# Kernel optimization log

Measured on AMD Instinct MI355X. Metric: run time of the kernel, lower is better.

Reference implementation:

```python
import jax, jax.numpy as jnp
import numpy as np

TRNA_N, DIS_N = 8000, 6000
D, H, E, B = 128, 256, 320000, 16384
NEG_SLOPE = 0.2  # gat_alpha
TEMP = 0.5


def _gat(src, tgt, s_idx, t_idx, Wsrc, Wtgt, a, n_src):
    # BipartiteGraphAttentionLayer (eval mode, dropout off)
    h_i = src @ Wsrc.T            # [n_src, D]
    h_j = tgt @ Wtgt.T            # [n_tgt, D]
    # cat([h_i[s], h_j[t]]) @ a == (h_i @ a[:D])[s] + (h_j @ a[D:])[t]
    s_i = h_i @ a[:D]             # [n_src]
    s_j = h_j @ a[D:]             # [n_tgt]
    e = jax.nn.leaky_relu(s_i[s_idx] + s_j[t_idx], NEG_SLOPE)
    e = jnp.clip(e, -30.0, 30.0)
    exp_e = jnp.exp(e)
    denom = jax.ops.segment_sum(exp_e, s_idx, num_segments=n_src)
    alpha = exp_e / (denom[s_idx] + 1e-8)
    out = jax.ops.segment_sum(h_j[t_idx] * alpha[:, None], s_idx, num_segments=n_src)
    return jax.nn.elu(out)


def _hg(x, S):
    # HCCF-style parameter-free hypergraph conv: nodes -> hyperedges -> nodes
    return jax.nn.elu(S @ (S.T @ x))


def _info_nce(z1, z2):
    z1 = z1 / (jnp.linalg.norm(z1, axis=1, keepdims=True) + 1e-12)
    z2 = z2 / (jnp.linalg.norm(z2, axis=1, keepdims=True) + 1e-12)
    sim = (z1 @ z2.T) / TEMP      # [N, N]
    logp = jax.nn.log_softmax(sim, axis=1)
    return -jnp.mean(jnp.diagonal(logp))


def setup_inputs():
    key = jax.random.key(0)
    ks = jax.random.split(key, 20)
    xn = lambda k, shp, sc: jax.random.normal(k, shp, dtype=jnp.float32) * sc
    d2 = (2.0 / (2 * D)) ** 0.5
    return dict(
        trna_embed=xn(ks[0], (TRNA_N, D), (2.0 / (TRNA_N + D)) ** 0.5),
        disease_embed=xn(ks[1], (DIS_N, D), (2.0 / (DIS_N + D)) ** 0.5),
        thyper=xn(ks[2], (D, H), (2.0 / (D + H)) ** 0.5),
        dhyper=xn(ks[3], (D, H), (2.0 / (D + H)) ** 0.5),
        gat_t_Wsrc=xn(ks[4], (3, D, D), d2),
        gat_t_Wtgt=xn(ks[5], (3, D, D), d2),
        gat_t_a=xn(ks[6], (3, 2 * D), 1.414 * (2.0 / (2 * D + 1)) ** 0.5),
        gat_d_Wsrc=xn(ks[7], (3, D, D), d2),
        gat_d_Wtgt=xn(ks[8], (3, D, D), d2),
        gat_d_a=xn(ks[9], (3, 2 * D), 1.414 * (2.0 / (2 * D + 1)) ** 0.5),
        mlp_W1=xn(ks[10], (D, 2 * D), (2.0 / (3 * D)) ** 0.5),
        mlp_b1=jnp.zeros((D,), jnp.float32),
        mlp_W2=xn(ks[11], (1, D), (2.0 / (D + 1)) ** 0.5),
        mlp_b2=jnp.zeros((1,), jnp.float32),
        gate_W=xn(ks[12], (1, D), (2.0 / (D + 1)) ** 0.5),
        gate_b=jnp.zeros((1,), jnp.float32),
        src_id=jax.random.randint(ks[13], (E,), 0, TRNA_N),
        tgt_id=jax.random.randint(ks[14], (E,), 0, DIS_N),
        trna_ids=jax.random.randint(ks[15], (B,), 0, TRNA_N),
        disease_ids=jax.random.randint(ks[16], (B,), 0, DIS_N),
    )


def reference(trna_embed, disease_embed, thyper, dhyper,
              gat_t_Wsrc, gat_t_Wtgt, gat_t_a,
              gat_d_Wsrc, gat_d_Wtgt, gat_d_a,
              mlp_W1, mlp_b1, mlp_W2, mlp_b2, gate_W, gate_b,
              src_id, tgt_id, trna_ids, disease_ids):
    # stage 1: simple-graph GAT pass
    sg_t = _gat(trna_embed, disease_embed, src_id, tgt_id,
                gat_t_Wsrc[0], gat_t_Wtgt[0], gat_t_a[0], TRNA_N)
    sg_d = _gat(disease_embed, sg_t, tgt_id, src_id,
                gat_d_Wsrc[0], gat_d_Wtgt[0], gat_d_a[0], DIS_N)
    # hypergraph passes 1-2
    hg_t = _hg(sg_t, sg_t @ thyper)
    hg_d = _hg(sg_d, sg_d @ dhyper)
    hg_t = _hg(hg_t, hg_t @ thyper)
    hg_d = _hg(hg_d, hg_d @ dhyper)
    # GAT layers 2-3 on hypergraph outputs
    sg_t = _gat(hg_t, hg_d, src_id, tgt_id,
                gat_t_Wsrc[1], gat_t_Wtgt[1], gat_t_a[1], TRNA_N)
    sg_d = _gat(hg_d, hg_t, tgt_id, src_id,
                gat_d_Wsrc[1], gat_d_Wtgt[1], gat_d_a[1], DIS_N)
    sg_t = _gat(sg_t, sg_d, src_id, tgt_id,
                gat_t_Wsrc[2], gat_t_Wtgt[2], gat_t_a[2], TRNA_N)
    sg_d = _gat(sg_d, sg_t, tgt_id, src_id,
                gat_d_Wsrc[2], gat_d_Wtgt[2], gat_d_a[2], DIS_N)
    # hypergraph pass 3
    hg_t = _hg(hg_t, hg_t @ thyper)
    hg_d = _hg(hg_d, hg_d @ dhyper)
    final_t = sg_t + hg_t
    final_d = sg_d + hg_d
    sel_t = final_t[trna_ids]
    sel_d = final_d[disease_ids]
    contrast = _info_nce(sg_t, hg_t) + _info_nce(sg_d, hg_d)
    gmf_vec = sel_t * sel_d
    gmf_pred = jnp.sum(gmf_vec, axis=-1)
    mlp_in = jnp.concatenate([sel_t, sel_d], axis=-1)
    h1 = jax.nn.relu(mlp_in @ mlp_W1.T + mlp_b1)
    mlp_pred = (h1 @ mlp_W2.T + mlp_b2)[:, 0]
    gate = jax.nn.sigmoid(gmf_vec @ gate_W.T + gate_b)[:, 0]
    fusion_pred = gate * gmf_pred + (1.0 - gate) * mlp_pred
    return (fusion_pred, sg_t, sg_d, gmf_pred, mlp_pred, contrast)
```

## Files before the change

### kernel.cpp

```cpp
#include <hip/hip_runtime.h>
#include <math.h>

#define N_T 8000
#define N_D 6000
#define N_E 320000
#define N_B 16384
#define NSTRIP 8

typedef __attribute__((ext_vector_type(8))) short s16x8;
typedef __attribute__((ext_vector_type(8))) __bf16 bf16x8;
typedef __attribute__((ext_vector_type(4))) float f32x4;

static __device__ __forceinline__ f32x4 mfma16(s16x8 a, s16x8 b, f32x4 c) {
  return __builtin_amdgcn_mfma_f32_16x16x32_bf16(
      __builtin_bit_cast(bf16x8, a), __builtin_bit_cast(bf16x8, b), c, 0, 0, 0);
}

static __device__ __forceinline__ unsigned short f2bf(float f) {
  unsigned u = __float_as_uint(f);
  u += 0x7FFF + ((u >> 16) & 1);
  return (unsigned short)(u >> 16);
}

static __device__ __forceinline__ float bf2f(unsigned short u) {
  return __uint_as_float(((unsigned)u) << 16);
}

__device__ __forceinline__ float wave_sum(float v) {
  v += __shfl_xor(v, 32, 64);
  v += __shfl_xor(v, 16, 64);
  v += __shfl_xor(v, 8, 64);
  v += __shfl_xor(v, 4, 64);
  v += __shfl_xor(v, 2, 64);
  v += __shfl_xor(v, 1, 64);
  return v;
}

__device__ __forceinline__ float half_sum(float v) {
  v += __shfl_xor(v, 16, 64);
  v += __shfl_xor(v, 8, 64);
  v += __shfl_xor(v, 4, 64);
  v += __shfl_xor(v, 2, 64);
  v += __shfl_xor(v, 1, 64);
  return v;
}

__global__ void k_hist2(const int* __restrict__ src, const int* __restrict__ tgt,
                        int* __restrict__ cnt) {
  int i = blockIdx.x * 256 + threadIdx.x;
  if (i < N_E) atomicAdd(&cnt[src[i]], 1);
  else if (i < 2 * N_E) atomicAdd(&cnt[N_T + tgt[i - N_E]], 1);
}

__global__ void k_scan2(const int* __restrict__ cnt, int* __restrict__ rp_t,
    int* __restrict__ cur_t, int* __restrict__ rp_d, int* __restrict__ cur_d) {
  const int* c = blockIdx.x ? cnt + N_T : cnt;
  const int n = blockIdx.x ? N_D : N_T;
  int* rp = blockIdx.x ? rp_d : rp_t;
  int* cur = blockIdx.x ? cur_d : cur_t;
  __shared__ int buf[1024];
  __shared__ int carry_s;
  if (threadIdx.x == 0) carry_s = 0;
  __syncthreads();
  for (int base = 0; base < n; base += 1024) {
    int c0 = carry_s;
    int i = base + (int)threadIdx.x;
    int v = (i < n) ? c[i] : 0;
    buf[threadIdx.x] = v;
    __syncthreads();
    for (int off = 1; off < 1024; off <<= 1) {
      int t = (threadIdx.x >= (unsigned)off) ? buf[threadIdx.x - off] : 0;
      __syncthreads();
      buf[threadIdx.x] += t;
      __syncthreads();
    }
    int incl = buf[threadIdx.x];
    if (i < n) { int e = c0 + incl - v; rp[i] = e; cur[i] = e; }
    __syncthreads();
    if (threadIdx.x == 0) carry_s = c0 + buf[1023];
    __syncthreads();
  }
  if (threadIdx.x == 0) rp[n] = carry_s;
}

__global__ void k_scatter2(const int* __restrict__ src, const int* __restrict__ tgt,
    int* __restrict__ cur_t, int* __restrict__ cur_d,
    int* __restrict__ nbr_t, int* __restrict__ nbr_d) {
  int i = blockIdx.x * 256 + threadIdx.x;
  if (i < N_E) {
    int p = atomicAdd(&cur_t[src[i]], 1);
    nbr_t[p] = tgt[i];
  } else if (i < 2 * N_E) {
    i -= N_E;
    int p = atomicAdd(&cur_d[tgt[i]], 1);
    nbr_d[p] = src[i];
  }
}

__global__ __launch_bounds__(256) void k_pgemm(const float* __restrict__ th,
    const float* __restrict__ dh, float* __restrict__ P_t, float* __restrict__ P_d) {
  const float* A = blockIdx.x < 4 ? th : dh;
  float* C = blockIdx.x < 4 ? P_t : P_d;
  const int sub = blockIdx.x & 3;
  const int row0 = (sub >> 1) * 64, col0 = (sub & 1) * 64;
  __shared__ float As[16][65];
  __shared__ float Bs[16][65];
  const int tid = threadIdx.x;
  const int tr = tid >> 4, tc = tid & 15;
  float acc[4][4] = {};
  for (int k0 = 0; k0 < 256; k0 += 16) {
    {
      int m = tid >> 2, kk = (tid & 3) * 4;
      float4 v = *(const float4*)(A + (size_t)(row0 + m) * 256 + k0 + kk);
      As[kk + 0][m] = v.x; As[kk + 1][m] = v.y; As[kk + 2][m] = v.z; As[kk + 3][m] = v.w;
    }
    {
      int nn = tid >> 2, kk = (tid & 3) * 4;
      float4 v = *(const float4*)(A + (size_t)(col0 + nn) * 256 + k0 + kk);
      Bs[kk + 0][nn] = v.x; Bs[kk + 1][nn] = v.y; Bs[kk + 2][nn] = v.z; Bs[kk + 3][nn] = v.w;
    }
    __syncthreads();
#pragma unroll
    for (int k = 0; k < 16; ++k) {
      float a[4], b[4];
#pragma unroll
      for (int i = 0; i < 4; ++i) a[i] = As[k][tr * 4 + i];
#pragma unroll
      for (int j = 0; j < 4; ++j) b[j] = Bs[k][tc * 4 + j];
#pragma unroll
      for (int i = 0; i < 4; ++i)
#pragma unroll
        for (int j = 0; j < 4; ++j)
          acc[i][j] = fmaf(a[i], b[j], acc[i][j]);
    }
    __syncthreads();
  }
#pragma unroll
  for (int i = 0; i < 4; ++i)
#pragma unroll
    for (int j = 0; j < 4; ++j)
      C[(size_t)(row0 + tr * 4 + i) * 128 + col0 + tc * 4 + j] = acc[i][j];
}

__global__ void k_tobf16m(const float* __restrict__ a0, unsigned short* __restrict__ y0,
    const float* __restrict__ a1, unsigned short* __restrict__ y1,
    const float* __restrict__ a2, unsigned short* __restrict__ y2,
    const float* __restrict__ a3, unsigned short* __restrict__ y3) {
  int i = blockIdx.x * 256 + threadIdx.x;
  const float* x; unsigned short* y;
  if (i < 12288) { x = a0; y = y0; }
  else if (i < 24576) { x = a1; y = y1; i -= 12288; }
  else if (i < 32768) { x = a2; y = y2; i -= 24576; }
  else if (i < 224768) { x = a3; y = y3; i -= 32768; }
  else return;
  float4 v = ((const float4*)x)[i];
  ushort4 o;
  o.x = f2bf(v.x); o.y = f2bf(v.y); o.z = f2bf(v.z); o.w = f2bf(v.w);
  ((ushort4*)y)[i] = o;
}

template<int K, int ACT, int BIAS, int SJMODE, int OUTF, int OUTB>
static __device__ __forceinline__ void mfma_body(
    const unsigned short* __restrict__ A, const unsigned short* __restrict__ B,
    const float* __restrict__ bias, const float* __restrict__ a2,
    float* __restrict__ Cf, unsigned short* __restrict__ Cb,
    float* __restrict__ sj_out, int M, int bx) {
  const int wave = threadIdx.x >> 6, lane = threadIdx.x & 63;
  const int row0 = bx * 32;
  const int col0 = wave * 32;
  const int l15 = lane & 15, kg = lane >> 4;
  constexpr int NS = K / 32;
  f32x4 acc[2][2] = {};
  s16x8 ab[2][2], bb[2][2];
  auto ld = [&](int buf, int k0) {
#pragma unroll
    for (int i = 0; i < 2; ++i) {
      int r = row0 + i * 16 + l15;
      ab[buf][i] = (r < M) ? *(const s16x8*)(A + (size_t)r * K + k0 + kg * 8) : (s16x8)0;
    }
#pragma unroll
    for (int j = 0; j < 2; ++j) {
      int c = col0 + j * 16 + l15;
      bb[buf][j] = *(const s16x8*)(B + (size_t)c * K + k0 + kg * 8);
    }
  };
  ld(0, 0);
#pragma unroll
  for (int s = 0; s < NS; ++s) {
    if (s + 1 < NS) ld((s + 1) & 1, (s + 1) * 32);
#pragma unroll
    for (int i = 0; i < 2; ++i)
#pragma unroll
      for (int j = 0; j < 2; ++j)
        acc[i][j] = mfma16(ab[s & 1][i], bb[s & 1][j], acc[i][j]);
  }
  __shared__ float sjl[4][32];
  float a2v[2];
  if (SJMODE) {
#pragma unroll
    for (int j = 0; j < 2; ++j) a2v[j] = a2[col0 + j * 16 + l15];
  }
#pragma unroll
  for (int i = 0; i < 2; ++i) {
    float part[4] = {0.f, 0.f, 0.f, 0.f};
#pragma unroll
    for (int j = 0; j < 2; ++j) {
      int gc = col0 + j * 16 + l15;
      float bv = BIAS ? bias[gc] : 0.f;
#pragma unroll
      for (int r = 0; r < 4; ++r) {
        int gr = row0 + i * 16 + kg * 4 + r;
        float v = acc[i][j][r] + bv;
        if (SJMODE == 1) part[r] += v * a2v[j];
        if (ACT == 1) v = v > 0.f ? v : __expf(v) - 1.f;
        if (ACT == 2) v = fmaxf(v, 0.f);
        if (SJMODE == 2) part[r] += v * a2v[j];
        if (gr < M) {
          if (OUTF) Cf[(size_t)gr * 128 + gc] = v;
          if (OUTB) Cb[(size_t)gr * 128 + gc] = f2bf(v);
        }
      }
    }
    if (SJMODE) {
#pragma unroll
      for (int r = 0; r < 4; ++r) {
        float p = part[r];
        p += __shfl_xor(p, 1, 64);
        p += __shfl_xor(p, 2, 64);
        p += __shfl_xor(p, 4, 64);
        p += __shfl_xor(p, 8, 64);
        if (l15 == 0) sjl[wave][i * 16 + kg * 4 + r] = p;
      }
    }
  }
  if (SJMODE) {
    __syncthreads();
    if (threadIdx.x < 32) {
      int gr = row0 + (int)threadIdx.x;
      if (gr < M)
        sj_out[gr] = sjl[0][threadIdx.x] + sjl[1][threadIdx.x] +
                     sjl[2][threadIdx.x] + sjl[3][threadIdx.x];
    }
  }
}

template<int K, int ACT, int BIAS, int SJMODE, int OUTF, int OUTB>
__global__ __launch_bounds__(256) void k_mfma(const unsigned short* __restrict__ A,
    const unsigned short* __restrict__ B, const float* __restrict__ bias,
    const float* __restrict__ a2, float* __restrict__ Cf, unsigned short* __restrict__ Cb,
    float* __restrict__ sj_out, int M) {
  mfma_body<K, ACT, BIAS, SJMODE, OUTF, OUTB>(A, B, bias, a2, Cf, Cb, sj_out, M, blockIdx.x);
}

template<int K, int ACT, int SJMODE, int OUTF, int OUTB>
__global__ __launch_bounds__(256) void k_mfma2(
    const unsigned short* __restrict__ A0, const unsigned short* __restrict__ B0,
    const float* __restrict__ a20, float* __restrict__ Cf0,
    unsigned short* __restrict__ Cb0, float* __restrict__ sj0, int M0, int G0,
    const unsigned short* __restrict__ A1, const unsigned short* __restrict__ B1,
    const float* __restrict__ a21, float* __restrict__ Cf1,
    unsigned short* __restrict__ Cb1, float* __restrict__ sj1, int M1) {
  int bx = blockIdx.x;
  if (bx < G0)
    mfma_body<K, ACT, 0, SJMODE, OUTF, OUTB>(A0, B0, nullptr, a20, Cf0, Cb0, sj0, M0, bx);
  else
    mfma_body<K, ACT, 0, SJMODE, OUTF, OUTB>(A1, B1, nullptr, a21, Cf1, Cb1, sj1, M1, bx - G0);
}

__global__ __launch_bounds__(256) void k_nce3(
    const unsigned short* __restrict__ z1t, const unsigned short* __restrict__ z2t,
    float* __restrict__ rs_tp,
    const unsigned short* __restrict__ z1d, const unsigned short* __restrict__ z2d,
    float* __restrict__ rs_dp) {
  __shared__ unsigned short bt[128 * 128];
  const int wave = threadIdx.x >> 6, lane = threadIdx.x & 63;
  const int l15 = lane & 15, kg = lane >> 4;
  int by = blockIdx.y;
  const unsigned short *z1, *z2; float* rowsum; int M, N;
  if (by < 63) { z1 = z1t; z2 = z2t; rowsum = rs_tp; M = N_T; N = N_T; }
  else { by -= 63; z1 = z1d; z2 = z2d; rowsum = rs_dp; M = N_D; N = N_D; }
  const int row0 = by * 128 + (wave >> 1) * 64;
  const int colw = (wave & 1) * 64;
  const int CT = (N + 127) >> 7;
  const int ctps = (CT + NSTRIP - 1) / NSTRIP;
  const int ct0 = blockIdx.x * ctps;
  const int ct1 = min(CT, ct0 + ctps);
  if (ct0 >= CT) return;
  s16x8 a[4][4];
#pragma unroll
  for (int ks = 0; ks < 4; ++ks)
#pragma unroll
    for (int i = 0; i < 4; ++i) {
      int r = row0 + i * 16 + l15;
      a[ks][i] = (r < M) ? *(const s16x8*)(z1 + (size_t)r * 128 + ks * 32 + kg * 8) : (s16x8)0;
    }
  float rs[4][4] = {};
  for (int ct = ct0; ct < ct1; ++ct) {
    const int cbase = ct * 128;
#pragma unroll
    for (int i = 0; i < 8; ++i) {
      int c = i * 256 + (int)threadIdx.x;
      int trow = c >> 4, ks = c & 15;
      int rg = cbase + trow;
      rg = rg < N ? rg : N - 1;
      s16x8 v = *(const s16x8*)(z2 + (size_t)rg * 128 + ks * 8);
      *(s16x8*)((char*)bt + trow * 256 + ((ks * 16) ^ ((trow & 7) << 4))) = v;
    }
    __syncthreads();
    f32x4 acc[4][4] = {};
#pragma unroll
    for (int ks = 0; ks < 4; ++ks) {
      s16x8 b[4];
#pragma unroll
      for (int j = 0; j < 4; ++j) {
        int trow = colw + j * 16 + l15;
        b[j] = *(const s16x8*)((const char*)bt + trow * 256 +
                               ((ks * 64 + kg * 16) ^ ((trow & 7) << 4)));
      }
#pragma unroll
      for (int i = 0; i < 4; ++i)
#pragma unroll
        for (int j = 0; j < 4; ++j)
          acc[i][j] = mfma16(a[ks][i], b[j], acc[i][j]);
    }
#pragma unroll
    for (int j = 0; j < 4; ++j) {
      int gc = cbase + colw + j * 16 + l15;
      bool cok = gc < N;
#pragma unroll
      for (int i = 0; i < 4; ++i)
#pragma unroll
        for (int r = 0; r < 4; ++r)
          if (cok) rs[i][r] += __expf(acc[i][j][r] * 2.0f);
    }
    __syncthreads();
  }
#pragma unroll
  for (int i = 0; i < 4; ++i)
#pragma unroll
    for (int r = 0; r < 4; ++r) {
      float v = rs[i][r];
      v += __shfl_xor(v, 1, 64);
      v += __shfl_xor(v, 2, 64);
      v += __shfl_xor(v, 4, 64);
      v += __shfl_xor(v, 8, 64);
      if (l15 == 0) {
        int gr = row0 + i * 16 + kg * 4 + r;
        if (gr < M) atomicAdd(&rowsum[gr], v);
      }
    }
}

__global__ __launch_bounds__(256) void k_syrk2m(const unsigned short* __restrict__ xbT,
    const unsigned short* __restrict__ xbD, float* __restrict__ partT,
    float* __restrict__ partD) {
  int b = blockIdx.x;
  const unsigned short* xb; float* part; int n;
  if (b < 128) { xb = xbT; part = partT + (size_t)b * 16384; n = N_T; }
  else { b -= 128; xb = xbD; part = partD + (size_t)b * 16384; n = N_D; }
  __shared__ float rows[4][128];
  int chunk = (n + 127) >> 7;
  int m0 = b * chunk, m1 = min(n, m0 + chunk);
  int tx = threadIdx.x & 15, ty = threadIdx.x >> 4;
  float acc[8][8] = {};
  for (int m = m0; m < m1; m += 4) {
    int nr = min(4, m1 - m);
    if ((int)threadIdx.x < nr * 64) {
      ushort2 u = ((const ushort2*)(xb + (size_t)m * 128))[threadIdx.x];
      rows[threadIdx.x >> 6][(threadIdx.x & 63) * 2] = bf2f(u.x);
      rows[threadIdx.x >> 6][(threadIdx.x & 63) * 2 + 1] = bf2f(u.y);
    }
    __syncthreads();
    for (int r = 0; r < nr; ++r) {
      float a[8], bv[8];
#pragma unroll
      for (int i = 0; i < 8; ++i) a[i] = rows[r][i * 16 + ty];
#pragma unroll
      for (int j = 0; j < 8; ++j) bv[j] = rows[r][j * 16 + tx];
#pragma unroll
      for (int i = 0; i < 8; ++i)
#pragma unroll
        for (int j = 0; j < 8; ++j)
          acc[i][j] = fmaf(a[i], bv[j], acc[i][j]);
    }
    __syncthreads();
  }
#pragma unroll
  for (int i = 0; i < 8; ++i)
#pragma unroll
    for (int j = 0; j < 8; ++j)
      part[(i * 16 + ty) * 128 + j * 16 + tx] = acc[i][j];
}

__global__ void k_redm(const float* __restrict__ partT, const float* __restrict__ partD,
                       float* __restrict__ GmT, float* __restrict__ GmD) {
  int b = blockIdx.x;
  const float* part = b < 64 ? partT : partD;
  float* G = b < 64 ? GmT : GmD;
  int i = (b & 63) * 256 + threadIdx.x;
  float s = 0.f;
  for (int c = 0; c < 128; ++c) s += part[(size_t)c * 16384 + i];
  G[i] = s;
}

__global__ __launch_bounds__(256) void k_wtm(const float* __restrict__ GmT,
    const float* __restrict__ P_t, unsigned short* __restrict__ wb_t,
    const float* __restrict__ GmD, const float* __restrict__ P_d,
    unsigned short* __restrict__ wb_d) {
  const float* G = blockIdx.x < 4 ? GmT : GmD;
  const float* P = blockIdx.x < 4 ? P_t : P_d;
  unsigned short* wb = blockIdx.x < 4 ? wb_t : wb_d;
  const int sub = blockIdx.x & 3;
  const int bi = sub >> 1, bj = sub & 1;
  __shared__ float Gs[64][129];
  __shared__ float Ps[128][65];
  for (int t = threadIdx.x; t < 8192; t += 256) {
    int il = t >> 7, k = t & 127;
    Gs[il][k] = G[(bi * 64 + il) * 128 + k];
    int pk = t >> 6, pj = t & 63;
    Ps[pk][pj] = P[pk * 128 + bj * 64 + pj];
  }
  __syncthreads();
  const int tx = threadIdx.x & 15, ty = threadIdx.x >> 4;
  float acc[4][4] = {};
  for (int k = 0; k < 128; ++k) {
    float a[4], b[4];
#pragma unroll
    for (int i = 0; i < 4; ++i) a[i] = Gs[ty * 4 + i][k];
#pragma unroll
    for (int j = 0; j < 4; ++j) b[j] = Ps[k][tx * 4 + j];
#pragma unroll
    for (int i = 0; i < 4; ++i)
#pragma unroll
      for (int j = 0; j < 4; ++j)
        acc[i][j] = fmaf(a[i], b[j], acc[i][j]);
  }
#pragma unroll
  for (int i = 0; i < 4; ++i)
#pragma unroll
    for (int j = 0; j < 4; ++j)
      wb[(bi * 64 + ty * 4 + i) * 128 + bj * 64 + tx * 4 + j] = f2bf(acc[i][j]);
}

__global__ void k_wvec6(const float* __restrict__ WsT, const float* __restrict__ aT,
                        const float* __restrict__ WsD, const float* __restrict__ aD,
                        float* __restrict__ wv) {
  int b = blockIdx.x, k = threadIdx.x;
  const float* W = b < 3 ? WsT + b * 16384 : WsD + (b - 3) * 16384;
  const float* a = b < 3 ? aT + b * 256 : aD + (b - 3) * 256;
  float s = 0.f;
  for (int n = 0; n < 128; ++n) s = fmaf(W[n * 128 + k], a[n], s);
  wv[b * 128 + k] = s;
}

__global__ void k_rowdot2(const float* __restrict__ trna, const float* __restrict__ dis,
    const float* __restrict__ wv, float* __restrict__ si_ta, float* __restrict__ si_da) {
  int r = blockIdx.x * 4 + (threadIdx.x >> 6);
  int lane = threadIdx.x & 63;
  const float* h; const float* a; float* o; int row;
  if (r < N_T) { h = trna; a = wv; o = si_ta; row = r; }
  else {
    row = r - N_T;
    if (row >= N_D) return;
    h = dis; a = wv + 3 * 128; o = si_da;
  }
  float2 v = *(const float2*)(h + (size_t)row * 128 + lane * 2);
  float2 av = *(const float2*)(a + lane * 2);
  float s = v.x * av.x + v.y * av.y;
  s = wave_sum(s);
  if (lane == 0) o[row] = s;
}

template<int OUTF, int OUTB, int EMIT_SI>
static __device__ __forceinline__ void agg_body(const int* __restrict__ rp,
    const int* __restrict__ nbr, const float* __restrict__ si,
    const float* __restrict__ sj, const unsigned short* __restrict__ hjb,
    float* __restrict__ outF, unsigned short* __restrict__ outB,
    const float* __restrict__ wv, float* __restrict__ si_out, int n, int bx) {
  int r = bx * 8 + ((int)threadIdx.x >> 5);
  int lane = threadIdx.x & 31;
  if (r >= n) return;
  int p0 = rp[r], p1 = rp[r + 1];
  float sir = si[r];
  int c4 = lane * 4;
  auto wcalc = [&](int t) {
    float v = sir + sj[t];
    v = v >= 0.f ? v : 0.2f * v;
    v = fminf(30.f, fmaxf(-30.f, v));
    return __expf(v);
  };
  float a0 = 0.f, a1 = 0.f, a2 = 0.f, a3 = 0.f, den = 0.f;
  int p = p0;
  for (; p + 4 <= p1; p += 4) {
    int t0 = nbr[p], t1 = nbr[p + 1], t2 = nbr[p + 2], t3 = nbr[p + 3];
    float w0 = wcalc(t0), w1 = wcalc(t1), w2 = wcalc(t2), w3 = wcalc(t3);
    ushort4 h0 = *(const ushort4*)(hjb + (size_t)t0 * 128 + c4);
    ushort4 h1 = *(const ushort4*)(hjb + (size_t)t1 * 128 + c4);
    ushort4 h2 = *(const ushort4*)(hjb + (size_t)t2 * 128 + c4);
    ushort4 h3 = *(const ushort4*)(hjb + (size_t)t3 * 128 + c4);
    den += (w0 + w1) + (w2 + w3);
    a0 += w0 * bf2f(h0.x) + w1 * bf2f(h1.x) + w2 * bf2f(h2.x) + w3 * bf2f(h3.x);
    a1 += w0 * bf2f(h0.y) + w1 * bf2f(h1.y) + w2 * bf2f(h2.y) + w3 * bf2f(h3.y);
    a2 += w0 * bf2f(h0.z) + w1 * bf2f(h1.z) + w2 * bf2f(h2.z) + w3 * bf2f(h3.z);
    a3 += w0 * bf2f(h0.w) + w1 * bf2f(h1.w) + w2 * bf2f(h2.w) + w3 * bf2f(h3.w);
  }
  for (; p < p1; ++p) {
    int t = nbr[p];
    float w = wcalc(t);
    ushort4 h = *(const ushort4*)(hjb + (size_t)t * 128 + c4);
    den += w;
    a0 += w * bf2f(h.x); a1 += w * bf2f(h.y);
    a2 += w * bf2f(h.z); a3 += w * bf2f(h.w);
  }
  float inv = 1.0f / (den + 1e-8f);
  float v0 = a0 * inv, v1 = a1 * inv, v2 = a2 * inv, v3 = a3 * inv;
  v0 = v0 > 0.f ? v0 : __expf(v0) - 1.f;
  v1 = v1 > 0.f ? v1 : __expf(v1) - 1.f;
  v2 = v2 > 0.f ? v2 : __expf(v2) - 1.f;
  v3 = v3 > 0.f ? v3 : __expf(v3) - 1.f;
  if (OUTF) {
    float4 of; of.x = v0; of.y = v1; of.z = v2; of.w = v3;
    *(float4*)(outF + (size_t)r * 128 + c4) = of;
  }
  if (OUTB) {
    ushort4 ob; ob.x = f2bf(v0); ob.y = f2bf(v1); ob.z = f2bf(v2); ob.w = f2bf(v3);
    *(ushort4*)(outB + (size_t)r * 128 + c4) = ob;
  }
  if (EMIT_SI) {
    float4 w4 = *(const float4*)(wv + c4);
    float d = v0 * w4.x + v1 * w4.y + v2 * w4.z + v3 * w4.w;
    d += __shfl_xor(d, 16, 64);
    d += __shfl_xor(d, 8, 64);
    d += __shfl_xor(d, 4, 64);
    d += __shfl_xor(d, 2, 64);
    d += __shfl_xor(d, 1, 64);
    if (lane == 0) si_out[r] = d;
  }
}

template<int OUTF, int OUTB, int EMIT_SI>
__global__ __launch_bounds__(256) void k_agg(const int* __restrict__ rp,
    const int* __restrict__ nbr, const float* __restrict__ si,
    const float* __restrict__ sj, const unsigned short* __restrict__ hjb,
    float* __restrict__ outF, unsigned short* __restrict__ outB,
    const float* __restrict__ wv, float* __restrict__ si_out, int n) {
  agg_body<OUTF, OUTB, EMIT_SI>(rp, nbr, si, sj, hjb, outF, outB, wv, si_out, n, blockIdx.x);
}

template<int OUTF, int OUTB, int EMIT_SI>
__global__ __launch_bounds__(256) void k_agg2(
    const int* __restrict__ rp0, const int* __restrict__ nbr0, const float* __restrict__ si0,
    const float* __restrict__ sj0, const unsigned short* __restrict__ hjb0,
    float* __restrict__ outF0, unsigned short* __restrict__ outB0,
    const float* __restrict__ wv0, float* __restrict__ sio0, int n0, int G0,
    const int* __restrict__ rp1, const int* __restrict__ nbr1, const float* __restrict__ si1,
    const float* __restrict__ sj1, const unsigned short* __restrict__ hjb1,
    float* __restrict__ outF1, unsigned short* __restrict__ outB1,
    const float* __restrict__ wv1, float* __restrict__ sio1, int n1) {
  int bx = blockIdx.x;
  if (bx < G0)
    agg_body<OUTF, OUTB, EMIT_SI>(rp0, nbr0, si0, sj0, hjb0, outF0, outB0, wv0, sio0, n0, bx);
  else
    agg_body<OUTF, OUTB, EMIT_SI>(rp1, nbr1, si1, sj1, hjb1, outF1, outB1, wv1, sio1, n1, bx - G0);
}

__global__ void k_norm2(const float* __restrict__ sgt, const float* __restrict__ hgt3,
    const float* __restrict__ sgd, const float* __restrict__ hgd3,
    unsigned short* __restrict__ z1t, unsigned short* __restrict__ z2t,
    unsigned short* __restrict__ z1d, unsigned short* __restrict__ z2d,
    float* __restrict__ rs_t, float* __restrict__ dg_t,
    float* __restrict__ rs_d, float* __restrict__ dg_d) {
  int ridx = blockIdx.x * 4 + (threadIdx.x >> 6);
  int lane = threadIdx.x & 63;
  const float *x1, *x2; unsigned short *o1, *o2; float *rs, *dg; int row;
  if (ridx < 8000) { x1 = sgt; x2 = hgt3; o1 = z1t; o2 = z2t; rs = rs_t; dg = dg_t; row = ridx; }
  else if (ridx < 14000) {
    row = ridx - 8000;
    x1 = sgd; x2 = hgd3; o1 = z1d; o2 = z2d; rs = rs_d; dg = dg_d;
  } else return;
  float2 v1 = *(const float2*)(x1 + (size_t)row * 128 + lane * 2);
  float2 v2 = *(const float2*)(x2 + (size_t)row * 128 + lane * 2);
  float ss1 = wave_sum(v1.x * v1.x + v1.y * v1.y);
  float ss2 = wave_sum(v2.x * v2.x + v2.y * v2.y);
  float i1 = 1.0f / (sqrtf(ss1) + 1e-12f);
  float i2 = 1.0f / (sqrtf(ss2) + 1e-12f);
  float n1x = v1.x * i1, n1y = v1.y * i1;
  float n2x = v2.x * i2, n2y = v2.y * i2;
  ushort2 w1; w1.x = f2bf(n1x); w1.y = f2bf(n1y);
  ushort2 w2; w2.x = f2bf(n2x); w2.y = f2bf(n2y);
  *(ushort2*)(o1 + (size_t)row * 128 + lane * 2) = w1;
  *(ushort2*)(o2 + (size_t)row * 128 + lane * 2) = w2;
  float d = wave_sum(n1x * n2x + n1y * n2y);
  if (lane == 0) { dg[row] = 2.0f * d; rs[row] = 0.f; }
}

__global__ void k_gather(const float* __restrict__ sgt, const float* __restrict__ hgt,
    const float* __restrict__ sgd, const float* __restrict__ hgd,
    const int* __restrict__ tids, const int* __restrict__ dids,
    const float* __restrict__ gateW, unsigned short* __restrict__ mlp_in_b,
    float* __restrict__ gmf, float* __restrict__ gate_lin, int nB) {
  int b = blockIdx.x * 4 + (threadIdx.x >> 6);
  int lane = threadIdx.x & 63;
  if (b >= nB) return;
  int ti = tids[b], di = dids[b];
  float2 a1 = *(const float2*)(sgt + (size_t)ti * 128 + lane * 2);
  float2 a2 = *(const float2*)(hgt + (size_t)ti * 128 + lane * 2);
  float2 c1 = *(const float2*)(sgd + (size_t)di * 128 + lane * 2);
  float2 c2 = *(const float2*)(hgd + (size_t)di * 128 + lane * 2);
  float2 st; st.x = a1.x + a2.x; st.y = a1.y + a2.y;
  float2 sd; sd.x = c1.x + c2.x; sd.y = c1.y + c2.y;
  ushort2 o1; o1.x = f2bf(st.x); o1.y = f2bf(st.y);
  ushort2 o2; o2.x = f2bf(sd.x); o2.y = f2bf(sd.y);
  *(ushort2*)(mlp_in_b + (size_t)b * 256 + lane * 2) = o1;
  *(ushort2*)(mlp_in_b + (size_t)b * 256 + 128 + lane * 2) = o2;
  float2 gv; gv.x = st.x * sd.x; gv.y = st.y * sd.y;
  float2 gw = *(const float2*)(gateW + lane * 2);
  float s1 = gv.x + gv.y;
  float s2 = gv.x * gw.x + gv.y * gw.y;
  s1 = wave_sum(s1);
  s2 = wave_sum(s2);
  if (lane == 0) { gmf[b] = s1; gate_lin[b] = s2; }
}

__global__ void k_final(const float* __restrict__ h1, const float* __restrict__ W2,
    const float* __restrict__ b2, const float* __restrict__ gate_lin,
    const float* __restrict__ gate_b, const float* __restrict__ gmf,
    float* __restrict__ fusion, float* __restrict__ mlp_pred, int nB) {
  int b = blockIdx.x * 4 + (threadIdx.x >> 6);
  int lane = threadIdx.x & 63;
  if (b >= nB) return;
  float2 hv = *(const float2*)(h1 + (size_t)b * 128 + lane * 2);
  float2 wv = *(const float2*)(W2 + lane * 2);
  float s = hv.x * wv.x + hv.y * wv.y;
  s = wave_sum(s);
  if (lane == 0) {
    float mp = s + b2[0];
    float g = 1.0f / (1.0f + __expf(-(gate_lin[b] + gate_b[0])));
    mlp_pred[b] = mp;
    fusion[b] = g * gmf[b] + (1.0f - g) * mp;
  }
}

__global__ void k_contrast(const float* __restrict__ rs_t, const float* __restrict__ dg_t,
    const float* __restrict__ rs_d, const float* __restrict__ dg_d, float* __restrict__ out) {
  __shared__ float red[256];
  float st = 0.f, sd = 0.f;
  for (int i = threadIdx.x; i < N_T; i += 256) st += __logf(rs_t[i]) - dg_t[i];
  for (int i = threadIdx.x; i < N_D; i += 256) sd += __logf(rs_d[i]) - dg_d[i];
  red[threadIdx.x] = st * (1.0f / N_T) + sd * (1.0f / N_D);
  __syncthreads();
  for (int off = 128; off; off >>= 1) {
    if (threadIdx.x < (unsigned)off) red[threadIdx.x] += red[threadIdx.x + off];
    __syncthreads();
  }
  if (threadIdx.x == 0) out[0] = red[0];
}

extern "C" void kernel_launch(void* const* d_in, const int* in_sizes, int n_in,
                              void* d_out, int out_size, void* d_ws, size_t ws_size,
                              hipStream_t stream) {
  const float* trna   = (const float*)d_in[0];
  const float* dis    = (const float*)d_in[1];
  const float* thyper = (const float*)d_in[2];
  const float* dhyper = (const float*)d_in[3];
  const float* WsrcT  = (const float*)d_in[4];
  const float* WtgtT  = (const float*)d_in[5];
  const float* aT     = (const float*)d_in[6];
  const float* WsrcD  = (const float*)d_in[7];
  const float* WtgtD  = (const float*)d_in[8];
  const float* aD     = (const float*)d_in[9];
  const float* W1     = (const float*)d_in[10];
  const float* b1     = (const float*)d_in[11];
  const float* W2     = (const float*)d_in[12];
  const float* b2     = (const float*)d_in[13];
  const float* gW     = (const float*)d_in[14];
  const float* gb     = (const float*)d_in[15];
  const int* src_id   = (const int*)d_in[16];
  const int* tgt_id   = (const int*)d_in[17];
  const int* tids     = (const int*)d_in[18];
  const int* dids     = (const int*)d_in[19];
  float* out = (float*)d_out;

  float* out_fusion = out;
  float* out_sgt    = out + 16384;
  float* out_sgd    = out + 16384 + 1024000;
  float* out_gmf    = out + 1808384;
  float* out_mlp    = out + 1824768;
  float* out_con    = out + 1841152;

  char* wsb = (char*)d_ws;
  size_t off = 0;
  auto alloc = [&](size_t bytes) -> void* {
    void* p = wsb + off;
    off += (bytes + 255) & ~(size_t)255;
    return p;
  };
  float* hg_t3  = (float*)alloc((size_t)N_T * 128 * 4);
  float* hg_d3  = (float*)alloc((size_t)N_D * 128 * 4);
  unsigned short* sgt_b  = (unsigned short*)alloc((size_t)N_T * 128 * 2);
  unsigned short* sgd_b  = (unsigned short*)alloc((size_t)N_D * 128 * 2);
  unsigned short* hgt_b  = (unsigned short*)alloc((size_t)N_T * 128 * 2);
  unsigned short* hgd_b  = (unsigned short*)alloc((size_t)N_D * 128 * 2);
  unsigned short* hgt2_b = (unsigned short*)alloc((size_t)N_T * 128 * 2);
  unsigned short* hgd2_b = (unsigned short*)alloc((size_t)N_D * 128 * 2);
  unsigned short* disb   = (unsigned short*)alloc((size_t)N_D * 128 * 2);
  unsigned short* hjbT   = (unsigned short*)alloc((size_t)N_T * 128 * 2);
  unsigned short* hjbD   = (unsigned short*)alloc((size_t)N_T * 128 * 2);
  unsigned short* zb1t = (unsigned short*)alloc((size_t)N_T * 128 * 2);
  unsigned short* zb2t = (unsigned short*)alloc((size_t)N_T * 128 * 2);
  unsigned short* zb1d = (unsigned short*)alloc((size_t)N_D * 128 * 2);
  unsigned short* zb2d = (unsigned short*)alloc((size_t)N_D * 128 * 2);
  unsigned short* wb_t = (unsigned short*)alloc(16384 * 2);
  unsigned short* wb_d = (unsigned short*)alloc(16384 * 2);
  unsigned short* wbT  = (unsigned short*)alloc(3 * 16384 * 2);
  unsigned short* wbD  = (unsigned short*)alloc(3 * 16384 * 2);
  unsigned short* W1b  = (unsigned short*)alloc(32768 * 2);
  unsigned short* mlp_in_b = (unsigned short*)alloc((size_t)N_B * 256 * 2);
  float* h1buf  = (float*)alloc((size_t)N_B * 128 * 4);
  float* partT  = (float*)mlp_in_b;
  float* partD  = partT + (size_t)128 * 16384;
  float* Gm_t   = (float*)alloc(16384 * 4);
  float* Gm_d   = (float*)alloc(16384 * 4);
  float* P_t    = (float*)alloc(16384 * 4);
  float* P_d    = (float*)alloc(16384 * 4);
  float* wvecs  = (float*)alloc(6 * 128 * 4);
  float* si_ta  = (float*)alloc(N_T * 4);
  float* si_tb  = (float*)alloc(N_T * 4);
  float* si_da  = (float*)alloc(N_D * 4);
  float* si_db  = (float*)alloc(N_D * 4);
  float* s_jT   = (float*)alloc(N_T * 4);
  float* s_jD   = (float*)alloc(N_T * 4);
  int* cnt      = (int*)alloc((N_T + N_D) * 4);
  int* rp_t     = (int*)alloc((N_T + 1) * 4);
  int* cur_t    = (int*)alloc(N_T * 4);
  int* rp_d     = (int*)alloc((N_D + 1) * 4);
  int* cur_d    = (int*)alloc(N_D * 4);
  int* nbrc_t   = (int*)alloc((size_t)N_E * 4);
  int* nbrc_d   = (int*)alloc((size_t)N_E * 4);
  float* rs_t   = (float*)alloc(N_T * 4);
  float* dg_t   = (float*)alloc(N_T * 4);
  float* rs_d   = (float*)alloc(N_D * 4);
  float* dg_d   = (float*)alloc(N_D * 4);
  float* g_lin  = (float*)alloc(N_B * 4);
  (void)ws_size; (void)in_sizes; (void)n_in; (void)out_size;

  const int gT32 = (N_T + 31) / 32;
  const int gD32 = (N_D + 31) / 32;
  const int aT8 = (N_T + 7) / 8, aD8 = (N_D + 7) / 8;

  hipMemsetAsync(cnt, 0, (N_T + N_D) * 4, stream);
  k_hist2<<<(2 * N_E + 255) / 256, 256, 0, stream>>>(src_id, tgt_id, cnt);
  k_scan2<<<2, 1024, 0, stream>>>(cnt, rp_t, cur_t, rp_d, cur_d);
  k_scatter2<<<(2 * N_E + 255) / 256, 256, 0, stream>>>(src_id, tgt_id, cur_t, cur_d,
      nbrc_t, nbrc_d);

  k_pgemm<<<8, 256, 0, stream>>>(thyper, dhyper, P_t, P_d);
  k_wvec6<<<6, 128, 0, stream>>>(WsrcT, aT, WsrcD, aD, wvecs);
  k_tobf16m<<<878, 256, 0, stream>>>(WtgtT, wbT, WtgtD, wbD, W1, W1b, dis, disb);
  k_rowdot2<<<(N_T + N_D + 3) / 4, 256, 0, stream>>>(trna, dis, wvecs, si_ta, si_da);

  k_mfma<128, 0, 0, 1, 0, 1><<<gD32, 256, 0, stream>>>(
      disb, wbT, nullptr, aT + 128, nullptr, hjbT, s_jT, N_D);
  k_agg<0, 1, 0><<<aT8, 256, 0, stream>>>(rp_t, nbrc_t, si_ta, s_jT, hjbT,
      nullptr, sgt_b, nullptr, nullptr, N_T);
  k_mfma<128, 0, 0, 1, 0, 1><<<gT32, 256, 0, stream>>>(
      sgt_b, wbD, nullptr, aD + 128, nullptr, hjbD, s_jD, N_T);
  k_agg<0, 1, 0><<<aD8, 256, 0, stream>>>(rp_d, nbrc_d, si_da, s_jD, hjbD,
      nullptr, sgd_b, nullptr, nullptr, N_D);

  k_syrk2m<<<256, 256, 0, stream>>>(sgt_b, sgd_b, partT, partD);
  k_redm<<<128, 256, 0, stream>>>(partT, partD, Gm_t, Gm_d);
  k_wtm<<<8, 256, 0, stream>>>(Gm_t, P_t, wb_t, Gm_d, P_d, wb_d);
  k_mfma2<128, 1, 0, 0, 1><<<gT32 + gD32, 256, 0, stream>>>(
      sgt_b, wb_t, nullptr, nullptr, hgt_b, nullptr, N_T, gT32,
      sgd_b, wb_d, nullptr, nullptr, hgd_b, nullptr, N_D);

  k_syrk2m<<<256, 256, 0, stream>>>(hgt_b, hgd_b, partT, partD);
  k_redm<<<128, 256, 0, stream>>>(partT, partD, Gm_t, Gm_d);
  k_wtm<<<8, 256, 0, stream>>>(Gm_t, P_t, wb_t, Gm_d, P_d, wb_d);
  k_mfma2<128, 1, 2, 0, 1><<<gT32 + gD32, 256, 0, stream>>>(
      hgt_b, wb_t, wvecs + 128, nullptr, hgt2_b, si_tb, N_T, gT32,
      hgd_b, wb_d, wvecs + 4 * 128, nullptr, hgd2_b, si_db, N_D);

  k_mfma2<128, 0, 1, 0, 1><<<gD32 + gT32, 256, 0, stream>>>(
      hgd2_b, wbT + 16384, aT + 256 + 128, nullptr, hjbT, s_jT, N_D, gD32,
      hgt2_b, wbD + 16384, aD + 256 + 128, nullptr, hjbD, s_jD, N_T);
  k_agg2<0, 1, 1><<<aT8 + aD8, 256, 0, stream>>>(
      rp_t, nbrc_t, si_tb, s_jT, hjbT, nullptr, sgt_b, wvecs + 2 * 128, si_ta, N_T, aT8,
      rp_d, nbrc_d, si_db, s_jD, hjbD, nullptr, sgd_b, wvecs + 5 * 128, si_da, N_D);

  k_mfma<128, 0, 0, 1, 0, 1><<<gD32, 256, 0, stream>>>(
      sgd_b, wbT + 32768, nullptr, aT + 512 + 128, nullptr, hjbT, s_jT, N_D);
  k_agg<1, 1, 0><<<aT8, 256, 0, stream>>>(rp_t, nbrc_t, si_ta, s_jT, hjbT,
      out_sgt, sgt_b, nullptr, nullptr, N_T);
  k_mfma<128, 0, 0, 1, 0, 1><<<gT32, 256, 0, stream>>>(
      sgt_b, wbD + 32768, nullptr, aD + 512 + 128, nullptr, hjbD, s_jD, N_T);
  k_agg<1, 0, 0><<<aD8, 256, 0, stream>>>(rp_d, nbrc_d, si_da, s_jD, hjbD,
      out_sgd, nullptr, nullptr, nullptr, N_D);

  k_syrk2m<<<256, 256, 0, stream>>>(hgt2_b, hgd2_b, partT, partD);
  k_redm<<<128, 256, 0, stream>>>(partT, partD, Gm_t, Gm_d);
  k_wtm<<<8, 256, 0, stream>>>(Gm_t, P_t, wb_t, Gm_d, P_d, wb_d);
  k_mfma2<128, 1, 0, 1, 0><<<gT32 + gD32, 256, 0, stream>>>(
      hgt2_b, wb_t, nullptr, hg_t3, nullptr, nullptr, N_T, gT32,
      hgd2_b, wb_d, nullptr, hg_d3, nullptr, nullptr, N_D);

  k_norm2<<<3500, 256, 0, stream>>>(out_sgt, hg_t3, out_sgd, hg_d3,
      zb1t, zb2t, zb1d, zb2d, rs_t, dg_t, rs_d, dg_d);
  k_nce3<<<dim3(NSTRIP, 63 + 47), 256, 0, stream>>>(
      zb1t, zb2t, rs_t, zb1d, zb2d, rs_d);
  k_contrast<<<1, 256, 0, stream>>>(rs_t, dg_t, rs_d, dg_d, out_con);

  k_gather<<<(N_B + 3) / 4, 256, 0, stream>>>(out_sgt, hg_t3, out_sgd, hg_d3,
      tids, dids, gW, mlp_in_b, out_gmf, g_lin, N_B);
  k_mfma<256, 2, 1, 0, 1, 0><<<N_B / 32, 256, 0, stream>>>(
      mlp_in_b, W1b, b1, nullptr, h1buf, nullptr, nullptr, N_B);
  k_final<<<(N_B + 3) / 4, 256, 0, stream>>>(h1buf, W2, b2, g_lin, gb,
      out_gmf, out_fusion, out_mlp, N_B);
}
```

Baseline: 488.2 us.

## Load InfoNCE B tiles directly into registers with double buffering, fold temperature scale

```diff
diff --git a/kernel.cpp b/kernel.cpp
--- a/kernel.cpp
+++ b/kernel.cpp
@@ -5,7 +5,7 @@
 #define N_D 6000
 #define N_E 320000
 #define N_B 16384
-#define NSTRIP 8
+#define NSTRIP 12
 
 typedef __attribute__((ext_vector_type(8))) short s16x8;
 typedef __attribute__((ext_vector_type(8))) __bf16 bf16x8;
@@ -28,15 +28,6 @@
 
 __device__ __forceinline__ float wave_sum(float v) {
   v += __shfl_xor(v, 32, 64);
-  v += __shfl_xor(v, 16, 64);
-  v += __shfl_xor(v, 8, 64);
-  v += __shfl_xor(v, 4, 64);
-  v += __shfl_xor(v, 2, 64);
-  v += __shfl_xor(v, 1, 64);
-  return v;
-}
-
-__device__ __forceinline__ float half_sum(float v) {
   v += __shfl_xor(v, 16, 64);
   v += __shfl_xor(v, 8, 64);
   v += __shfl_xor(v, 4, 64);
@@ -267,12 +258,11 @@
     mfma_body<K, ACT, 0, SJMODE, OUTF, OUTB>(A1, B1, nullptr, a21, Cf1, Cb1, sj1, M1, bx - G0);
 }
 
-__global__ __launch_bounds__(256) void k_nce3(
+__global__ __launch_bounds__(256) void k_nce4(
     const unsigned short* __restrict__ z1t, const unsigned short* __restrict__ z2t,
     float* __restrict__ rs_tp,
     const unsigned short* __restrict__ z1d, const unsigned short* __restrict__ z2d,
     float* __restrict__ rs_dp) {
-  __shared__ unsigned short bt[128 * 128];
   const int wave = threadIdx.x >> 6, lane = threadIdx.x & 63;
   const int l15 = lane & 15, kg = lane >> 4;
   int by = blockIdx.y;
@@ -285,7 +275,8 @@
   const int ctps = (CT + NSTRIP - 1) / NSTRIP;
   const int ct0 = blockIdx.x * ctps;
   const int ct1 = min(CT, ct0 + ctps);
-  if (ct0 >= CT) return;
+  const int nct = ct1 - ct0;
+  if (nct <= 0) return;
   s16x8 a[4][4];
 #pragma unroll
   for (int ks = 0; ks < 4; ++ks)
@@ -294,46 +285,43 @@
       int r = row0 + i * 16 + l15;
       a[ks][i] = (r < M) ? *(const s16x8*)(z1 + (size_t)r * 128 + ks * 32 + kg * 8) : (s16x8)0;
     }
+  s16x8 b[2][4];
+  auto ldb = [&](int buf, int ct, int ks) {
+    const unsigned short* base = z2 + (size_t)(ct * 128 + colw) * 128 + ks * 32 + kg * 8;
+#pragma unroll
+    for (int j = 0; j < 4; ++j)
+      b[buf][j] = *(const s16x8*)(base + (size_t)(j * 16 + l15) * 128);
+  };
   float rs[4][4] = {};
-  for (int ct = ct0; ct < ct1; ++ct) {
-    const int cbase = ct * 128;
-#pragma unroll
-    for (int i = 0; i < 8; ++i) {
-      int c = i * 256 + (int)threadIdx.x;
-      int trow = c >> 4, ks = c & 15;
-      int rg = cbase + trow;
-      rg = rg < N ? rg : N - 1;
-      s16x8 v = *(const s16x8*)(z2 + (size_t)rg * 128 + ks * 8);
-      *(s16x8*)((char*)bt + trow * 256 + ((ks * 16) ^ ((trow & 7) << 4))) = v;
-    }
-    __syncthreads();
+  int cs = by % nct;
+  ldb(0, ct0 + cs, 0);
+  for (int cc = 0; cc < nct; ++cc) {
+    const int ct = ct0 + cs;
+    const int csn = (cs + 1 == nct) ? 0 : cs + 1;
     f32x4 acc[4][4] = {};
 #pragma unroll
     for (int ks = 0; ks < 4; ++ks) {
-      s16x8 b[4];
-#pragma unroll
-      for (int j = 0; j < 4; ++j) {
-        int trow = colw + j * 16 + l15;
-        b[j] = *(const s16x8*)((const char*)bt + trow * 256 +
-                               ((ks * 64 + kg * 16) ^ ((trow & 7) << 4)));
+      if (ks < 3) ldb((ks + 1) & 1, ct, ks + 1);
+      else if (cc + 1 < nct) ldb(0, ct0 + csn, 0);
+#pragma unroll
+      for (int i = 0; i < 4; ++i)
+#pragma unroll
+        for (int j = 0; j < 4; ++j)
+          acc[i][j] = mfma16(a[ks][i], b[ks & 1][j], acc[i][j]);
+    }
+    const int c0 = ct * 128 + colw;
+#pragma unroll
+    for (int j = 0; j < 4; ++j) {
+      bool cok = c0 + j * 16 + l15 < N;
+      if (cok) {
+#pragma unroll
+        for (int i = 0; i < 4; ++i)
+#pragma unroll
+          for (int r = 0; r < 4; ++r)
+            rs[i][r] += __expf(acc[i][j][r]);
       }
-#pragma unroll
-      for (int i = 0; i < 4; ++i)
-#pragma unroll
-        for (int j = 0; j < 4; ++j)
-          acc[i][j] = mfma16(a[ks][i], b[j], acc[i][j]);
-    }
-#pragma unroll
-    for (int j = 0; j < 4; ++j) {
-      int gc = cbase + colw + j * 16 + l15;
-      bool cok = gc < N;
-#pragma unroll
-      for (int i = 0; i < 4; ++i)
-#pragma unroll
-        for (int r = 0; r < 4; ++r)
-          if (cok) rs[i][r] += __expf(acc[i][j][r] * 2.0f);
-    }
-    __syncthreads();
+    }
+    cs = csn;
   }
 #pragma unroll
   for (int i = 0; i < 4; ++i)
@@ -491,6 +479,29 @@
   };
   float a0 = 0.f, a1 = 0.f, a2 = 0.f, a3 = 0.f, den = 0.f;
   int p = p0;
+  for (; p + 8 <= p1; p += 8) {
+    int t0 = nbr[p], t1 = nbr[p + 1], t2 = nbr[p + 2], t3 = nbr[p + 3];
+    int t4 = nbr[p + 4], t5 = nbr[p + 5], t6 = nbr[p + 6], t7 = nbr[p + 7];
+    float w0 = wcalc(t0), w1 = wcalc(t1), w2 = wcalc(t2), w3 = wcalc(t3);
+    float w4 = wcalc(t4), w5 = wcalc(t5), w6 = wcalc(t6), w7 = wcalc(t7);
+    ushort4 h0 = *(const ushort4*)(hjb + (size_t)t0 * 128 + c4);
+    ushort4 h1 = *(const ushort4*)(hjb + (size_t)t1 * 128 + c4);
+    ushort4 h2 = *(const ushort4*)(hjb + (size_t)t2 * 128 + c4);
+    ushort4 h3 = *(const ushort4*)(hjb + (size_t)t3 * 128 + c4);
+    ushort4 h4 = *(const ushort4*)(hjb + (size_t)t4 * 128 + c4);
+    ushort4 h5 = *(const ushort4*)(hjb + (size_t)t5 * 128 + c4);
+    ushort4 h6 = *(const ushort4*)(hjb + (size_t)t6 * 128 + c4);
+    ushort4 h7 = *(const ushort4*)(hjb + (size_t)t7 * 128 + c4);
+    den += ((w0 + w1) + (w2 + w3)) + ((w4 + w5) + (w6 + w7));
+    a0 += (w0 * bf2f(h0.x) + w1 * bf2f(h1.x) + w2 * bf2f(h2.x) + w3 * bf2f(h3.x)) +
+          (w4 * bf2f(h4.x) + w5 * bf2f(h5.x) + w6 * bf2f(h6.x) + w7 * bf2f(h7.x));
+    a1 += (w0 * bf2f(h0.y) + w1 * bf2f(h1.y) + w2 * bf2f(h2.y) + w3 * bf2f(h3.y)) +
+          (w4 * bf2f(h4.y) + w5 * bf2f(h5.y) + w6 * bf2f(h6.y) + w7 * bf2f(h7.y));
+    a2 += (w0 * bf2f(h0.z) + w1 * bf2f(h1.z) + w2 * bf2f(h2.z) + w3 * bf2f(h3.z)) +
+          (w4 * bf2f(h4.z) + w5 * bf2f(h5.z) + w6 * bf2f(h6.z) + w7 * bf2f(h7.z));
+    a3 += (w0 * bf2f(h0.w) + w1 * bf2f(h1.w) + w2 * bf2f(h2.w) + w3 * bf2f(h3.w)) +
+          (w4 * bf2f(h4.w) + w5 * bf2f(h5.w) + w6 * bf2f(h6.w) + w7 * bf2f(h7.w));
+  }
   for (; p + 4 <= p1; p += 4) {
     int t0 = nbr[p], t1 = nbr[p + 1], t2 = nbr[p + 2], t3 = nbr[p + 3];
     float w0 = wcalc(t0), w1 = wcalc(t1), w2 = wcalc(t2), w3 = wcalc(t3);
@@ -586,7 +597,7 @@
   float i2 = 1.0f / (sqrtf(ss2) + 1e-12f);
   float n1x = v1.x * i1, n1y = v1.y * i1;
   float n2x = v2.x * i2, n2y = v2.y * i2;
-  ushort2 w1; w1.x = f2bf(n1x); w1.y = f2bf(n1y);
+  ushort2 w1; w1.x = f2bf(n1x + n1x); w1.y = f2bf(n1y + n1y);
   ushort2 w2; w2.x = f2bf(n2x); w2.y = f2bf(n2y);
   *(ushort2*)(o1 + (size_t)row * 128 + lane * 2) = w1;
   *(ushort2*)(o2 + (size_t)row * 128 + lane * 2) = w2;
@@ -707,9 +718,9 @@
   unsigned short* hjbT   = (unsigned short*)alloc((size_t)N_T * 128 * 2);
   unsigned short* hjbD   = (unsigned short*)alloc((size_t)N_T * 128 * 2);
   unsigned short* zb1t = (unsigned short*)alloc((size_t)N_T * 128 * 2);
-  unsigned short* zb2t = (unsigned short*)alloc((size_t)N_T * 128 * 2);
+  unsigned short* zb2t = (unsigned short*)alloc((size_t)(N_T + 128) * 128 * 2);
   unsigned short* zb1d = (unsigned short*)alloc((size_t)N_D * 128 * 2);
-  unsigned short* zb2d = (unsigned short*)alloc((size_t)N_D * 128 * 2);
+  unsigned short* zb2d = (unsigned short*)alloc((size_t)(N_D + 128) * 128 * 2);
   unsigned short* wb_t = (unsigned short*)alloc(16384 * 2);
   unsigned short* wb_d = (unsigned short*)alloc(16384 * 2);
   unsigned short* wbT  = (unsigned short*)alloc(3 * 16384 * 2);
@@ -807,7 +818,7 @@
 
   k_norm2<<<3500, 256, 0, stream>>>(out_sgt, hg_t3, out_sgd, hg_d3,
       zb1t, zb2t, zb1d, zb2d, rs_t, dg_t, rs_d, dg_d);
-  k_nce3<<<dim3(NSTRIP, 63 + 47), 256, 0, stream>>>(
+  k_nce4<<<dim3(NSTRIP, 63 + 47), 256, 0, stream>>>(
       zb1t, zb2t, rs_t, zb1d, zb2d, rs_d);
   k_contrast<<<1, 256, 0, stream>>>(rs_t, dg_t, rs_d, dg_d, out_con);
 
```

After: 479.6 us. About the same (-1.7%).
